# Performance work log

Measured on AMD Instinct MI355X. Metric: run time of the kernel, lower is better.

## Reference

```python
import jax, jax.numpy as jnp
import numpy as np

B, L, D = 4, 2048, 256
MAX_NGRAM = 3
SLOTS = 64


def setup_inputs() -> dict:
    key = jax.random.key(0)
    k1, k2, k3 = jax.random.split(key, 3)
    x = jax.random.normal(k1, (B, L, D), dtype=jnp.float32)
    memory = jax.random.normal(k2, (SLOTS, MAX_NGRAM, D), dtype=jnp.float32)
    pos_bias = jax.random.normal(k3, (SLOTS, MAX_NGRAM), dtype=jnp.float32)
    return {"x": x, "memory": memory, "pos_bias": pos_bias}


def _extract_ngrams(x, max_ngram):
    # Left-pad with max_ngram-1 zero vectors, then take max_ngram shifted views.
    b, l, d = x.shape
    xpad = jnp.concatenate([jnp.zeros((b, max_ngram - 1, d), x.dtype), x], axis=1)
    # ngrams[b, l, n] = xpad[b, n + l]  -> (B, L, N, d)
    return jnp.stack([xpad[:, n:n + l] for n in range(max_ngram)], axis=2)


def reference(x, memory, pos_bias):
    slots, max_ngram, d = memory.shape
    ngrams = _extract_ngrams(x, max_ngram)                      # (B, L, N, d)
    # Contraction over d replaces the huge (B,L,M,N,d) broadcast-multiply.
    sims = jnp.einsum('blnd,mnd->blmn', ngrams, memory)         # (B, L, M, N)
    scores = sims + pos_bias[None, None]                        # (B, L, M, N)
    best = jnp.argmax(scores, axis=-1)                          # (B, L, M) int
    # selected[b,l,m] = memory[m, best[b,l,m]]  -> (B, L, M, d)
    selected = memory[jnp.arange(slots)[None, None, :], best]
    return selected.sum(axis=2)                                 # (B, L, d)
```

## Files before the change

kernel.cpp:

```cpp
#include <hip/hip_runtime.h>
#include <stdint.h>

#define LL   2048
#define DD   256
#define SLOTS 64
#define MN   192
#define PT   8192

typedef _Float16 half8 __attribute__((ext_vector_type(8)));
typedef float    f32x4 __attribute__((ext_vector_type(4)));

#define FRAG_ELEMS (MN * DD)

__global__ __launch_bounds__(256) void prep_kernel(
    const float* __restrict__ mem,
    _Float16* __restrict__ aS_h, _Float16* __restrict__ aS_l,
    _Float16* __restrict__ bG_h)
{
    const int e = blockIdx.x * 256 + threadIdx.x;
    const int mn = e >> 8;
    const int d  = e & 255;
    const float v = mem[e];
    const _Float16 h  = (_Float16)v;
    const _Float16 lo = (_Float16)(v - (float)h);

    {
        const int tm = mn >> 4, r = mn & 15;
        const int c = d >> 5, q = (d >> 3) & 3, j = d & 7;
        const int i1 = ((tm * 8 + c) * 64 + (q * 16 + r)) * 8 + j;
        aS_h[i1] = h; aS_l[i1] = lo;
    }
    {
        const int c2 = mn >> 5, q2 = (mn >> 3) & 3, j2 = mn & 7;
        const int td = d >> 4, n2 = d & 15;
        const int i2 = ((td * 6 + c2) * 64 + (q2 * 16 + n2)) * 8 + j2;
        bG_h[i2] = h;
    }
}

__global__ __launch_bounds__(256) void fused_kernel(
    const float* __restrict__ x, const float* __restrict__ bias,
    const _Float16* __restrict__ aS_h, const _Float16* __restrict__ aS_l,
    const _Float16* __restrict__ bG_h,
    float* __restrict__ out)
{
    __shared__ _Float16 xfh[2 * 8 * 64 * 8];
    __shared__ _Float16 xfl[2 * 8 * 64 * 8];
    __shared__ float    scores[MN * 18];
    __shared__ float    biasS[MN];
    __shared__ uint32_t selS[16 * 8];

    const int p0   = blockIdx.x * 16;
    const int tid  = threadIdx.x;
    const int lane = tid & 63;
    const int w    = tid >> 6;
    const int q    = lane >> 4, col = lane & 15;

    half8 ah[2][3], al[2][3];
#pragma unroll
    for (int i = 0; i < 3; ++i) {
        const int tm = w * 3 + i;
        const size_t off = (size_t)((tm * 8 + 0) * 64 + lane) * 8;
        ah[0][i] = *(const half8*)(aS_h + off);
        al[0][i] = *(const half8*)(aS_l + off);
    }

    if (tid < 128) selS[tid] = 0u;
    if (tid < MN)  biasS[tid] = bias[tid];

    {
        const int c  = tid & 7;
        const int rr = tid >> 3;
        int g = p0 - 2 + rr;
        g = g < 0 ? 0 : (g > PT - 1 ? PT - 1 : g);
        const float4* xr = (const float4*)(x + (size_t)g * DD + c * 32);
        const int pt = rr >> 4, lr = rr & 15;
#pragma unroll
        for (int qq = 0; qq < 4; ++qq) {
            const float4 u = xr[qq * 2];
            const float4 v = xr[qq * 2 + 1];
            float f[8] = {u.x, u.y, u.z, u.w, v.x, v.y, v.z, v.w};
            half8 hi, lo;
#pragma unroll
            for (int j = 0; j < 8; ++j) {
                const _Float16 h = (_Float16)f[j];
                hi[j] = h;
                lo[j] = (_Float16)(f[j] - (float)h);
            }
            const int base = ((pt * 8 + c) * 64 + qq * 16 + lr) * 8;
            *(half8*)(xfh + base) = hi;
            *(half8*)(xfl + base) = lo;
        }
    }
    __syncthreads();

    {
        f32x4 acc[3][2];
#pragma unroll
        for (int i = 0; i < 3; ++i)
#pragma unroll
            for (int p = 0; p < 2; ++p) acc[i][p] = (f32x4){0.f, 0.f, 0.f, 0.f};

        half8 bh[2][2], bl[2][2];
#pragma unroll
        for (int p = 0; p < 2; ++p) {
            const int base = ((p * 8 + 0) * 64 + lane) * 8;
            bh[0][p] = *(const half8*)(xfh + base);
            bl[0][p] = *(const half8*)(xfl + base);
        }

#pragma unroll
        for (int c = 0; c < 8; ++c) {
            const int cur = c & 1, nxt = cur ^ 1;
            if (c < 7) {
#pragma unroll
                for (int i = 0; i < 3; ++i) {
                    const int tm = w * 3 + i;
                    const size_t off = (size_t)((tm * 8 + c + 1) * 64 + lane) * 8;
                    ah[nxt][i] = *(const half8*)(aS_h + off);
                    al[nxt][i] = *(const half8*)(aS_l + off);
                }
#pragma unroll
                for (int p = 0; p < 2; ++p) {
                    const int base = ((p * 8 + c + 1) * 64 + lane) * 8;
                    bh[nxt][p] = *(const half8*)(xfh + base);
                    bl[nxt][p] = *(const half8*)(xfl + base);
                }
            }
#pragma unroll
            for (int i = 0; i < 3; ++i)
#pragma unroll
                for (int p = 0; p < 2; ++p) {
                    acc[i][p] = __builtin_amdgcn_mfma_f32_16x16x32_f16(ah[cur][i], bh[cur][p], acc[i][p], 0, 0, 0);
                    acc[i][p] = __builtin_amdgcn_mfma_f32_16x16x32_f16(ah[cur][i], bl[cur][p], acc[i][p], 0, 0, 0);
                    acc[i][p] = __builtin_amdgcn_mfma_f32_16x16x32_f16(al[cur][i], bh[cur][p], acc[i][p], 0, 0, 0);
                }
        }

#pragma unroll
        for (int i = 0; i < 3; ++i) {
            const int tm = w * 3 + i;
#pragma unroll
            for (int p = 0; p < 2; ++p) {
                const int wp = p * 16 + col;
                if (wp < 18) {
#pragma unroll
                    for (int r = 0; r < 4; ++r)
                        scores[(tm * 16 + q * 4 + r) * 18 + wp] = acc[i][p][r];
                }
            }
        }
    }

    half8 mg[2][4];
#pragma unroll
    for (int i = 0; i < 4; ++i) {
        const int td = w * 4 + i;
        const size_t off = (size_t)((td * 6 + 0) * 64 + lane) * 8;
        mg[0][i] = *(const half8*)(bG_h + off);
    }
    __syncthreads();

#pragma unroll
    for (int it = 0; it < 4; ++it) {
        const int t2 = tid + it * 256;
        const int pl = t2 & 15;
        const int m  = t2 >> 4;
        const int p  = p0 + pl;
        const int l  = p & (LL - 1);
        const float v0 = ((l >= 2) ? scores[(3 * m + 0) * 18 + pl + 0] : 0.f) + biasS[3 * m + 0];
        const float v1 = ((l >= 1) ? scores[(3 * m + 1) * 18 + pl + 1] : 0.f) + biasS[3 * m + 1];
        const float v2 =              scores[(3 * m + 2) * 18 + pl + 2]       + biasS[3 * m + 2];
        int bn = 0; float bv = v0;
        if (v1 > bv) { bv = v1; bn = 1; }
        if (v2 > bv) { bv = v2; bn = 2; }
        const int mnb = 3 * m + bn;
        atomicOr(&selS[pl * 8 + (mnb >> 5)], 1u << (mnb & 31));
    }
    __syncthreads();

    {
        uint32_t sw[6];
#pragma unroll
        for (int c = 0; c < 6; ++c) sw[c] = selS[col * 8 + c];

        f32x4 acc2[4];
#pragma unroll
        for (int i = 0; i < 4; ++i) acc2[i] = (f32x4){0.f, 0.f, 0.f, 0.f};

        const _Float16 ONE = (_Float16)1.f, ZERO = (_Float16)0.f;
        const int qb = q * 8;
#pragma unroll
        for (int c = 0; c < 6; ++c) {
            const int cur = c & 1, nxt = cur ^ 1;
            if (c < 5) {
#pragma unroll
                for (int i = 0; i < 4; ++i) {
                    const int td = w * 4 + i;
                    const size_t off = (size_t)((td * 6 + c + 1) * 64 + lane) * 8;
                    mg[nxt][i] = *(const half8*)(bG_h + off);
                }
            }
            half8 sel;
#pragma unroll
            for (int j = 0; j < 8; ++j)
                sel[j] = ((sw[c] >> (qb + j)) & 1u) ? ONE : ZERO;
#pragma unroll
            for (int i = 0; i < 4; ++i)
                acc2[i] = __builtin_amdgcn_mfma_f32_16x16x32_f16(sel, mg[cur][i], acc2[i], 0, 0, 0);
        }

#pragma unroll
        for (int i = 0; i < 4; ++i) {
            const int td = w * 4 + i;
#pragma unroll
            for (int r = 0; r < 4; ++r)
                out[(size_t)(p0 + q * 4 + r) * DD + td * 16 + col] = acc2[i][r];
        }
    }
}

extern "C" void kernel_launch(void* const* d_in, const int* in_sizes, int n_in,
                              void* d_out, int out_size, void* d_ws, size_t ws_size,
                              hipStream_t stream) {
    (void)in_sizes; (void)n_in; (void)out_size; (void)ws_size;
    const float* x    = (const float*)d_in[0];
    const float* mem  = (const float*)d_in[1];
    const float* bias = (const float*)d_in[2];
    float* out = (float*)d_out;

    _Float16* aS_h = (_Float16*)d_ws;
    _Float16* aS_l = aS_h + FRAG_ELEMS;
    _Float16* bG_h = aS_l + FRAG_ELEMS;

    prep_kernel<<<FRAG_ELEMS / 256, 256, 0, stream>>>(mem, aS_h, aS_l, bG_h);
    fused_kernel<<<PT / 16, 256, 0, stream>>>(x, bias, aS_h, aS_l, bG_h, out);
}
```

Measured before the change: 76.63 us.

## Double block threads, permute memory rows n-major, replace atomics with ballots

The fused kernel now runs 512 threads per block. The score GEMM is split across two position-tile groups and four slot groups, and the gather GEMM is split across eight waves with two d-tiles each. The prep kernel reorders memory rows as n-major (n*64+m), so each wave's lane maps to one slot. The argmax selection bitmask can then be built with three wave ballots instead of shared-memory atomicOr. The score stride is padded to 19 to reduce bank conflicts. Per-wave register use drops, in exchange for more waves per block and more redundant A-fragment loads across position groups.

```diff
diff --git a/kernel.cpp b/kernel.cpp
--- a/kernel.cpp
+++ b/kernel.cpp
@@ -18,35 +18,36 @@
     _Float16* __restrict__ bG_h)
 {
     const int e = blockIdx.x * 256 + threadIdx.x;
-    const int mn = e >> 8;
-    const int d  = e & 255;
-    const float v = mem[e];
+    const int mnp = e >> 8;
+    const int d   = e & 255;
+    const int n = mnp >> 6, m = mnp & 63;
+    const float v = mem[((m * 3 + n) << 8) + d];
     const _Float16 h  = (_Float16)v;
     const _Float16 lo = (_Float16)(v - (float)h);
 
     {
-        const int tm = mn >> 4, r = mn & 15;
+        const int tm = mnp >> 4, r = mnp & 15;
         const int c = d >> 5, q = (d >> 3) & 3, j = d & 7;
         const int i1 = ((tm * 8 + c) * 64 + (q * 16 + r)) * 8 + j;
         aS_h[i1] = h; aS_l[i1] = lo;
     }
     {
-        const int c2 = mn >> 5, q2 = (mn >> 3) & 3, j2 = mn & 7;
+        const int c2 = mnp >> 5, q2 = (mnp >> 3) & 3, j2 = mnp & 7;
         const int td = d >> 4, n2 = d & 15;
         const int i2 = ((td * 6 + c2) * 64 + (q2 * 16 + n2)) * 8 + j2;
         bG_h[i2] = h;
     }
 }
 
-__global__ __launch_bounds__(256) void fused_kernel(
+__global__ __launch_bounds__(512, 4) void fused_kernel(
     const float* __restrict__ x, const float* __restrict__ bias,
     const _Float16* __restrict__ aS_h, const _Float16* __restrict__ aS_l,
     const _Float16* __restrict__ bG_h,
     float* __restrict__ out)
 {
-    __shared__ _Float16 xfh[2 * 8 * 64 * 8];
-    __shared__ _Float16 xfl[2 * 8 * 64 * 8];
-    __shared__ float    scores[MN * 18];
+    __shared__ __align__(16) _Float16 xfh[2 * 8 * 64 * 8];
+    __shared__ __align__(16) _Float16 xfl[2 * 8 * 64 * 8];
+    __shared__ float    scores[MN * 19];
     __shared__ float    biasS[MN];
     __shared__ uint32_t selS[16 * 8];
 
@@ -55,39 +56,44 @@
     const int lane = tid & 63;
     const int w    = tid >> 6;
     const int q    = lane >> 4, col = lane & 15;
+    const int pg   = w >> 2;
+    const int tmg  = w & 3;
 
     half8 ah[2][3], al[2][3];
 #pragma unroll
     for (int i = 0; i < 3; ++i) {
-        const int tm = w * 3 + i;
+        const int tm = tmg * 3 + i;
         const size_t off = (size_t)((tm * 8 + 0) * 64 + lane) * 8;
         ah[0][i] = *(const half8*)(aS_h + off);
         al[0][i] = *(const half8*)(aS_l + off);
     }
 
-    if (tid < 128) selS[tid] = 0u;
-    if (tid < MN)  biasS[tid] = bias[tid];
-
-    {
-        const int c  = tid & 7;
-        const int rr = tid >> 3;
+    if (tid < MN) {
+        const int m = tid & 63, n = tid >> 6;
+        biasS[tid] = bias[m * 3 + n];
+    }
+
+    {
+        const int rr = tid >> 4;
+        const int dc = tid & 15;
         int g = p0 - 2 + rr;
         g = g < 0 ? 0 : (g > PT - 1 ? PT - 1 : g);
-        const float4* xr = (const float4*)(x + (size_t)g * DD + c * 32);
+        const float4* xr = (const float4*)(x + (size_t)g * DD + dc * 16);
         const int pt = rr >> 4, lr = rr & 15;
-#pragma unroll
-        for (int qq = 0; qq < 4; ++qq) {
-            const float4 u = xr[qq * 2];
-            const float4 v = xr[qq * 2 + 1];
+        const int c  = dc >> 1, h = dc & 1;
+#pragma unroll
+        for (int s = 0; s < 2; ++s) {
+            const float4 u = xr[s * 2];
+            const float4 v = xr[s * 2 + 1];
             float f[8] = {u.x, u.y, u.z, u.w, v.x, v.y, v.z, v.w};
             half8 hi, lo;
 #pragma unroll
             for (int j = 0; j < 8; ++j) {
-                const _Float16 h = (_Float16)f[j];
-                hi[j] = h;
-                lo[j] = (_Float16)(f[j] - (float)h);
-            }
-            const int base = ((pt * 8 + c) * 64 + qq * 16 + lr) * 8;
+                const _Float16 hh = (_Float16)f[j];
+                hi[j] = hh;
+                lo[j] = (_Float16)(f[j] - (float)hh);
+            }
+            const int base = ((pt * 8 + c) * 64 + (2 * h + s) * 16 + lr) * 8;
             *(half8*)(xfh + base) = hi;
             *(half8*)(xfl + base) = lo;
         }
@@ -95,18 +101,15 @@
     __syncthreads();
 
     {
-        f32x4 acc[3][2];
-#pragma unroll
-        for (int i = 0; i < 3; ++i)
-#pragma unroll
-            for (int p = 0; p < 2; ++p) acc[i][p] = (f32x4){0.f, 0.f, 0.f, 0.f};
-
-        half8 bh[2][2], bl[2][2];
-#pragma unroll
-        for (int p = 0; p < 2; ++p) {
-            const int base = ((p * 8 + 0) * 64 + lane) * 8;
-            bh[0][p] = *(const half8*)(xfh + base);
-            bl[0][p] = *(const half8*)(xfl + base);
+        f32x4 acc[3];
+#pragma unroll
+        for (int i = 0; i < 3; ++i) acc[i] = (f32x4){0.f, 0.f, 0.f, 0.f};
+
+        half8 bh[2], bl[2];
+        {
+            const int base = ((pg * 8 + 0) * 64 + lane) * 8;
+            bh[0] = *(const half8*)(xfh + base);
+            bl[0] = *(const half8*)(xfl + base);
         }
 
 #pragma unroll
@@ -115,67 +118,63 @@
             if (c < 7) {
 #pragma unroll
                 for (int i = 0; i < 3; ++i) {
-                    const int tm = w * 3 + i;
+                    const int tm = tmg * 3 + i;
                     const size_t off = (size_t)((tm * 8 + c + 1) * 64 + lane) * 8;
                     ah[nxt][i] = *(const half8*)(aS_h + off);
                     al[nxt][i] = *(const half8*)(aS_l + off);
                 }
-#pragma unroll
-                for (int p = 0; p < 2; ++p) {
-                    const int base = ((p * 8 + c + 1) * 64 + lane) * 8;
-                    bh[nxt][p] = *(const half8*)(xfh + base);
-                    bl[nxt][p] = *(const half8*)(xfl + base);
-                }
-            }
-#pragma unroll
-            for (int i = 0; i < 3; ++i)
-#pragma unroll
-                for (int p = 0; p < 2; ++p) {
-                    acc[i][p] = __builtin_amdgcn_mfma_f32_16x16x32_f16(ah[cur][i], bh[cur][p], acc[i][p], 0, 0, 0);
-                    acc[i][p] = __builtin_amdgcn_mfma_f32_16x16x32_f16(ah[cur][i], bl[cur][p], acc[i][p], 0, 0, 0);
-                    acc[i][p] = __builtin_amdgcn_mfma_f32_16x16x32_f16(al[cur][i], bh[cur][p], acc[i][p], 0, 0, 0);
-                }
-        }
-
+                const int base = ((pg * 8 + c + 1) * 64 + lane) * 8;
+                bh[nxt] = *(const half8*)(xfh + base);
+                bl[nxt] = *(const half8*)(xfl + base);
+            }
+#pragma unroll
+            for (int i = 0; i < 3; ++i) {
+                acc[i] = __builtin_amdgcn_mfma_f32_16x16x32_f16(ah[cur][i], bh[cur], acc[i], 0, 0, 0);
+                acc[i] = __builtin_amdgcn_mfma_f32_16x16x32_f16(ah[cur][i], bl[cur], acc[i], 0, 0, 0);
+                acc[i] = __builtin_amdgcn_mfma_f32_16x16x32_f16(al[cur][i], bh[cur], acc[i], 0, 0, 0);
+            }
+        }
+
+        const int wp = pg * 16 + col;
 #pragma unroll
         for (int i = 0; i < 3; ++i) {
-            const int tm = w * 3 + i;
-#pragma unroll
-            for (int p = 0; p < 2; ++p) {
-                const int wp = p * 16 + col;
-                if (wp < 18) {
-#pragma unroll
-                    for (int r = 0; r < 4; ++r)
-                        scores[(tm * 16 + q * 4 + r) * 18 + wp] = acc[i][p][r];
-                }
-            }
-        }
-    }
-
-    half8 mg[2][4];
-#pragma unroll
-    for (int i = 0; i < 4; ++i) {
-        const int td = w * 4 + i;
+            const int tm = tmg * 3 + i;
+            if (wp < 18) {
+#pragma unroll
+                for (int r = 0; r < 4; ++r)
+                    scores[(tm * 16 + q * 4 + r) * 19 + wp] = acc[i][r];
+            }
+        }
+    }
+
+    half8 mg[2][2];
+#pragma unroll
+    for (int i = 0; i < 2; ++i) {
+        const int td = w * 2 + i;
         const size_t off = (size_t)((td * 6 + 0) * 64 + lane) * 8;
         mg[0][i] = *(const half8*)(bG_h + off);
     }
     __syncthreads();
 
 #pragma unroll
-    for (int it = 0; it < 4; ++it) {
-        const int t2 = tid + it * 256;
-        const int pl = t2 & 15;
-        const int m  = t2 >> 4;
+    for (int it = 0; it < 2; ++it) {
+        const int pl = w * 2 + it;
+        const int m  = lane;
         const int p  = p0 + pl;
         const int l  = p & (LL - 1);
-        const float v0 = ((l >= 2) ? scores[(3 * m + 0) * 18 + pl + 0] : 0.f) + biasS[3 * m + 0];
-        const float v1 = ((l >= 1) ? scores[(3 * m + 1) * 18 + pl + 1] : 0.f) + biasS[3 * m + 1];
-        const float v2 =              scores[(3 * m + 2) * 18 + pl + 2]       + biasS[3 * m + 2];
+        const float v0 = ((l >= 2) ? scores[(      m) * 19 + pl + 0] : 0.f) + biasS[      m];
+        const float v1 = ((l >= 1) ? scores[( 64 + m) * 19 + pl + 1] : 0.f) + biasS[ 64 + m];
+        const float v2 =             scores[(128 + m) * 19 + pl + 2]        + biasS[128 + m];
         int bn = 0; float bv = v0;
         if (v1 > bv) { bv = v1; bn = 1; }
         if (v2 > bv) { bv = v2; bn = 2; }
-        const int mnb = 3 * m + bn;
-        atomicOr(&selS[pl * 8 + (mnb >> 5)], 1u << (mnb & 31));
+        const unsigned long long b0 = __ballot(bn == 0);
+        const unsigned long long b1 = __ballot(bn == 1);
+        const unsigned long long b2 = __ballot(bn == 2);
+        if (lane < 6) {
+            const unsigned long long B = (lane >> 1) == 0 ? b0 : ((lane >> 1) == 1 ? b1 : b2);
+            selS[pl * 8 + lane] = (uint32_t)(B >> ((lane & 1) * 32));
+        }
     }
     __syncthreads();
 
@@ -184,9 +183,9 @@
 #pragma unroll
         for (int c = 0; c < 6; ++c) sw[c] = selS[col * 8 + c];
 
-        f32x4 acc2[4];
-#pragma unroll
-        for (int i = 0; i < 4; ++i) acc2[i] = (f32x4){0.f, 0.f, 0.f, 0.f};
+        f32x4 acc2[2];
+#pragma unroll
+        for (int i = 0; i < 2; ++i) acc2[i] = (f32x4){0.f, 0.f, 0.f, 0.f};
 
         const _Float16 ONE = (_Float16)1.f, ZERO = (_Float16)0.f;
         const int qb = q * 8;
@@ -195,8 +194,8 @@
             const int cur = c & 1, nxt = cur ^ 1;
             if (c < 5) {
 #pragma unroll
-                for (int i = 0; i < 4; ++i) {
-                    const int td = w * 4 + i;
+                for (int i = 0; i < 2; ++i) {
+                    const int td = w * 2 + i;
                     const size_t off = (size_t)((td * 6 + c + 1) * 64 + lane) * 8;
                     mg[nxt][i] = *(const half8*)(bG_h + off);
                 }
@@ -206,13 +205,13 @@
             for (int j = 0; j < 8; ++j)
                 sel[j] = ((sw[c] >> (qb + j)) & 1u) ? ONE : ZERO;
 #pragma unroll
-            for (int i = 0; i < 4; ++i)
+            for (int i = 0; i < 2; ++i)
                 acc2[i] = __builtin_amdgcn_mfma_f32_16x16x32_f16(sel, mg[cur][i], acc2[i], 0, 0, 0);
         }
 
 #pragma unroll
-        for (int i = 0; i < 4; ++i) {
-            const int td = w * 4 + i;
+        for (int i = 0; i < 2; ++i) {
+            const int td = w * 2 + i;
 #pragma unroll
             for (int r = 0; r < 4; ++r)
                 out[(size_t)(p0 + q * 4 + r) * DD + td * 16 + col] = acc2[i][r];
@@ -234,5 +233,5 @@
     _Float16* bG_h = aS_l + FRAG_ELEMS;
 
     prep_kernel<<<FRAG_ELEMS / 256, 256, 0, stream>>>(mem, aS_h, aS_l, bG_h);
-    fused_kernel<<<PT / 16, 256, 0, stream>>>(x, bias, aS_h, aS_l, bG_h, out);
+    fused_kernel<<<PT / 16, 512, 0, stream>>>(x, bias, aS_h, aS_l, bG_h, out);
 }
```

Measured after the change: 78.61 us. 1.03x slower.
